# Optimization experiments

Measured on AMD Instinct MI355X. Metric: run time of the kernel, lower is better.

The kernel has to match this reference:

```python
import jax, jax.numpy as jnp
import numpy as np

NUM_HEADS = 32
NUM_KV_HEADS = 8
HEAD_DIM = 64
HIDDEN = 2048
EPS = 1e-05
ROPE_THETA = 1000000.0


def _rmsnorm(x, w):
    # x: [..., head_dim]
    var = jnp.mean(x * x, axis=-1, keepdims=True)
    return w * (x * jax.lax.rsqrt(var + EPS))


def _rope(q, k):
    # q,k: [B, h, T, d]
    T, d = q.shape[2], q.shape[3]
    inv_freq = 1.0 / (ROPE_THETA ** (jnp.arange(0, d, 2, dtype=jnp.float32) / d))
    t = jnp.arange(T, dtype=jnp.float32)
    freqs = jnp.outer(t, inv_freq)               # [T, d/2]
    emb = jnp.concatenate([freqs, freqs], -1)    # [T, d]
    cos = jnp.cos(emb)[None, None].astype(q.dtype)
    sin = jnp.sin(emb)[None, None].astype(q.dtype)

    def rotate(x):
        x1, x2 = x[..., : d // 2], x[..., d // 2 :]
        return jnp.concatenate([-x2, x1], -1)

    return q * cos + rotate(q) * sin, k * cos + rotate(k) * sin


def setup_inputs() -> dict:
    key = jax.random.key(0)
    ks = jax.random.split(key, 7)
    s = 0.02
    x = jax.random.normal(ks[0], (2, 2048, HIDDEN), jnp.float32)
    Wq = jax.random.normal(ks[1], (HIDDEN, NUM_HEADS * HEAD_DIM), jnp.float32) * s
    Wk = jax.random.normal(ks[2], (HIDDEN, NUM_KV_HEADS * HEAD_DIM), jnp.float32) * s
    Wv = jax.random.normal(ks[3], (HIDDEN, NUM_KV_HEADS * HEAD_DIM), jnp.float32) * s
    Wo = jax.random.normal(ks[4], (NUM_HEADS * HEAD_DIM, HIDDEN), jnp.float32) * s
    q_ln_w = jnp.ones((HEAD_DIM,), jnp.float32)
    k_ln_w = jnp.ones((HEAD_DIM,), jnp.float32)
    return {"x": x, "Wq": Wq, "Wk": Wk, "Wv": Wv, "Wo": Wo, "q_ln_w": q_ln_w, "k_ln_w": k_ln_w}


def reference(x, Wq, Wk, Wv, Wo, q_ln_w, k_ln_w):
    B, T, _ = x.shape
    g = NUM_HEADS // NUM_KV_HEADS  # GQA groups = 4
    q = (x @ Wq).reshape(B, T, NUM_HEADS, HEAD_DIM)
    k = (x @ Wk).reshape(B, T, NUM_KV_HEADS, HEAD_DIM)
    v = (x @ Wv).reshape(B, T, NUM_KV_HEADS, HEAD_DIM)
    q = _rmsnorm(q, q_ln_w)
    k = _rmsnorm(k, k_ln_w)
    q = q.transpose(0, 2, 1, 3)  # [B, nh, T, d]
    k = k.transpose(0, 2, 1, 3)  # [B, nkv, T, d]
    v = v.transpose(0, 2, 1, 3)
    q, k = _rope(q, k)
    # native GQA: fold query heads into (kv_head, group) without repeating K/V
    qg = q.reshape(B, NUM_KV_HEADS, g, T, HEAD_DIM)
    scale = 1.0 / jnp.sqrt(jnp.array(HEAD_DIM, q.dtype))
    scores = jnp.einsum("bkgtd,bksd->bkgts", qg, k) * scale  # [B,nkv,g,T,T]
    causal = jnp.tril(jnp.ones((T, T), bool))
    scores = jnp.where(causal, scores, jnp.finfo(scores.dtype).min)
    probs = jax.nn.softmax(scores, axis=-1)
    out = jnp.einsum("bkgts,bksd->bkgtd", probs, v)  # [B,nkv,g,T,d]
    out = out.reshape(B, NUM_HEADS, T, HEAD_DIM).transpose(0, 2, 1, 3).reshape(B, T, -1)
    return out @ Wo
```

## Files before the change

kernel.cpp:

```cpp
#include <hip/hip_runtime.h>
#include <cstdint>
#include <cstddef>

typedef unsigned short u16;
typedef __attribute__((ext_vector_type(8))) short short8;
typedef __attribute__((ext_vector_type(4))) short short4v;
typedef __attribute__((ext_vector_type(4))) float float4v;
typedef __attribute__((ext_vector_type(4))) unsigned short ushort4v;
typedef __attribute__((ext_vector_type(2))) float float2v;

__device__ __forceinline__ u16 f2bf(float f) {
    union { float f; uint32_t u; } x; x.f = f;
    uint32_t r = x.u + 0x7fffu + ((x.u >> 16) & 1u);
    return (u16)(r >> 16);
}
__device__ __forceinline__ uint32_t pack_bf16x2(float lo, float hi) {
    union { float f; uint32_t u; } a, b; a.f = lo; b.f = hi;
    return __builtin_amdgcn_perm(b.u + 0x8000u, a.u + 0x8000u, 0x07060302u);
}
__device__ __forceinline__ void gl_lds16(const u16* g, u16* l) {
    __builtin_amdgcn_global_load_lds(
        (const __attribute__((address_space(1))) void*)g,
        (__attribute__((address_space(3))) void*)l, 16, 0, 0);
}

__global__ __launch_bounds__(256) void prep(const float4v* __restrict__ x,
                                            const float* __restrict__ Wq,
                                            const float* __restrict__ Wk,
                                            const float* __restrict__ Wv,
                                            const float* __restrict__ Wo,
                                            ushort4v* __restrict__ xb,
                                            u16* __restrict__ wqkv_t,
                                            u16* __restrict__ wo_t,
                                            float2v* __restrict__ tab) {
    __shared__ float lds[32][33];
    const int bid = blockIdx.x;
    const int tid = threadIdx.x;
    if (bid < 8192) {
        const int i = bid * 256 + tid;
        float4v v = x[i];
        ushort4v o;
        #pragma unroll
        for (int j = 0; j < 4; ++j) o[j] = f2bf(v[j]);
        xb[i] = o;
        return;
    }
    if (bid < 8448) {
        const int idx = (bid - 8192) * 256 + tid;
        const int t = idx >> 5;
        const int i = idx & 31;
        const float invf = exp2f(-(float)i * (19.931568569324174f / 32.0f));
        float sv, cv;
        sincosf((float)t * invf, &sv, &cv);
        float2v o; o[0] = cv; o[1] = sv;
        tab[idx] = o;
        return;
    }
    const float* src;
    int Ns, n0, k0, scol0;
    u16* dst;
    if (bid < 14592) {
        const int id = bid - 8448;
        const int bx = id % 96, by = id / 96;
        n0 = bx * 32; k0 = by * 32;
        if (n0 < 2048)      { src = Wq; Ns = 2048; scol0 = n0; }
        else if (n0 < 2560) { src = Wk; Ns = 512;  scol0 = n0 - 2048; }
        else                { src = Wv; Ns = 512;  scol0 = n0 - 2560; }
        dst = wqkv_t;
    } else {
        const int id = bid - 14592;
        const int bx = id & 63, by = id >> 6;
        n0 = bx * 32; k0 = by * 32;
        src = Wo; Ns = 2048; scol0 = n0;
        dst = wo_t;
    }
    const int row = tid >> 3;
    const int c4  = (tid & 7) * 4;
    const float4v v = *(const float4v*)(src + (size_t)(k0 + row) * Ns + scol0 + c4);
    #pragma unroll
    for (int i = 0; i < 4; ++i) lds[row][c4 + i] = v[i];
    __syncthreads();
    const int nrow = tid >> 3;
    const int k4   = (tid & 7) * 4;
    ushort4v o;
    #pragma unroll
    for (int i = 0; i < 4; ++i) o[i] = f2bf(lds[k4 + i][nrow]);
    *(ushort4v*)(dst + (size_t)(n0 + nrow) * 2048 + k0 + k4) = o;
}

__global__ __launch_bounds__(256, 3) void gemm_bt(const u16* __restrict__ A,
                                                  const u16* __restrict__ Bt,
                                                  float* __restrict__ C,
                                                  int M, int N, int K) {
    __shared__ u16 lds_a[128 * 32];
    __shared__ u16 lds_b[128 * 32];
    const int tid  = threadIdx.x;
    const int wave = tid >> 6;
    const int lane = tid & 63;
    const int quad = lane >> 4;
    const int l15  = lane & 15;
    const long m0 = (long)blockIdx.x * 128;
    const long n0 = (long)blockIdx.y * 128;
    const int wm = (wave >> 1) * 64;
    const int wn = (wave & 1) * 64;
    const int s_row = tid >> 2;
    const int s_col = (tid & 3) * 8;

    float4v acc[4][4];
    #pragma unroll
    for (int i = 0; i < 4; ++i)
        #pragma unroll
        for (int j = 0; j < 4; ++j)
            #pragma unroll
            for (int r = 0; r < 4; ++r) acc[i][j][r] = 0.0f;

    const u16* ga0 = A  + (m0 + s_row) * (long)K + s_col;
    const u16* ga1 = ga0 + 64 * (long)K;
    const u16* gb0 = Bt + (n0 + s_row) * (long)K + s_col;
    const u16* gb1 = gb0 + 64 * (long)K;
    u16* la = lds_a + tid * 8;
    u16* lb = lds_b + tid * 8;

    const int n_k = K >> 5;
    for (int it = 0; it < n_k; ++it) {
        const int k0 = it << 5;
        gl_lds16(ga0 + k0, la);
        gl_lds16(ga1 + k0, la + 2048);
        gl_lds16(gb0 + k0, lb);
        gl_lds16(gb1 + k0, lb + 2048);
        __syncthreads();
        short8 af[4], bfr[4];
        #pragma unroll
        for (int mt = 0; mt < 4; ++mt)
            af[mt] = *(const short8*)(lds_a + (wm + mt * 16 + l15) * 32 + quad * 8);
        #pragma unroll
        for (int nt = 0; nt < 4; ++nt)
            bfr[nt] = *(const short8*)(lds_b + (wn + nt * 16 + l15) * 32 + quad * 8);
        #pragma unroll
        for (int mt = 0; mt < 4; ++mt)
            #pragma unroll
            for (int nt = 0; nt < 4; ++nt)
                acc[mt][nt] = __builtin_amdgcn_mfma_f32_16x16x32_bf16(af[mt], bfr[nt], acc[mt][nt], 0, 0, 0);
        __syncthreads();
    }
    #pragma unroll
    for (int mt = 0; mt < 4; ++mt) {
        #pragma unroll
        for (int nt = 0; nt < 4; ++nt) {
            const long gr = m0 + wm + mt * 16 + quad * 4;
            const long gc = n0 + wn + nt * 16 + l15;
            #pragma unroll
            for (int r = 0; r < 4; ++r)
                C[(gr + r) * N + gc] = acc[mt][nt][r];
        }
    }
}

__global__ __launch_bounds__(256, 3) void gemm_qkv(const u16* __restrict__ A,
                                                   const u16* __restrict__ Bt,
                                                   const float* __restrict__ qw,
                                                   const float* __restrict__ kw,
                                                   const float2v* __restrict__ tab,
                                                   u16* __restrict__ Qr,
                                                   u16* __restrict__ Kr,
                                                   u16* __restrict__ Vt) {
    const int K = 2048;
    __shared__ u16 lds_a[128 * 32];
    __shared__ u16 lds_b[128 * 32];
    const int tid  = threadIdx.x;
    const int wave = tid >> 6;
    const int lane = tid & 63;
    const int quad = lane >> 4;
    const int l15  = lane & 15;
    const long m0 = (long)blockIdx.x * 128;
    const long n0 = (long)blockIdx.y * 128;
    const int wm = (wave >> 1) * 64;
    const int wn = (wave & 1) * 64;
    const int s_row = tid >> 2;
    const int s_col = (tid & 3) * 8;

    float4v acc[4][4];
    #pragma unroll
    for (int i = 0; i < 4; ++i)
        #pragma unroll
        for (int j = 0; j < 4; ++j)
            #pragma unroll
            for (int r = 0; r < 4; ++r) acc[i][j][r] = 0.0f;

    const u16* ga0 = A  + (m0 + s_row) * (long)K + s_col;
    const u16* ga1 = ga0 + 64 * (long)K;
    const u16* gb0 = Bt + (n0 + s_row) * (long)K + s_col;
    const u16* gb1 = gb0 + 64 * (long)K;
    u16* la = lds_a + tid * 8;
    u16* lb = lds_b + tid * 8;

    const int n_k = K >> 5;
    for (int it = 0; it < n_k; ++it) {
        const int k0 = it << 5;
        gl_lds16(ga0 + k0, la);
        gl_lds16(ga1 + k0, la + 2048);
        gl_lds16(gb0 + k0, lb);
        gl_lds16(gb1 + k0, lb + 2048);
        __syncthreads();
        short8 af[4], bfr[4];
        #pragma unroll
        for (int mt = 0; mt < 4; ++mt)
            af[mt] = *(const short8*)(lds_a + (wm + mt * 16 + l15) * 32 + quad * 8);
        #pragma unroll
        for (int nt = 0; nt < 4; ++nt)
            bfr[nt] = *(const short8*)(lds_b + (wn + nt * 16 + l15) * 32 + quad * 8);
        #pragma unroll
        for (int mt = 0; mt < 4; ++mt)
            #pragma unroll
            for (int nt = 0; nt < 4; ++nt)
                acc[mt][nt] = __builtin_amdgcn_mfma_f32_16x16x32_bf16(af[mt], bfr[nt], acc[mt][nt], 0, 0, 0);
        __syncthreads();
    }

    const int col0 = (int)n0 + wn;
    if (col0 < 2560) {
        const bool isQ = (col0 < 2048);
        const float* lw = isQ ? qw : kw;
        float wreg[4];
        #pragma unroll
        for (int nt = 0; nt < 4; ++nt) wreg[nt] = lw[nt * 16 + l15];
        const float qs = isQ ? 0.18033688011112042f : 1.0f;
        u16* dst = isQ ? (Qr + ((size_t)(col0 >> 6)) * 2048 * 64)
                       : (Kr + ((size_t)((col0 - 2048) >> 6)) * 2048 * 64);
        const size_t head_stride = isQ ? ((size_t)32 * 2048 * 64) : ((size_t)8 * 2048 * 64);
        #pragma unroll
        for (int mt = 0; mt < 4; ++mt) {
            const int gr0 = (int)m0 + wm + mt * 16 + quad * 4;
            const int b = gr0 >> 11, tt0 = gr0 & 2047;
            float rms[4];
            #pragma unroll
            for (int r = 0; r < 4; ++r) {
                float s = 0.0f;
                #pragma unroll
                for (int nt = 0; nt < 4; ++nt) s += acc[mt][nt][r] * acc[mt][nt][r];
                s += __shfl_xor(s, 1);
                s += __shfl_xor(s, 2);
                s += __shfl_xor(s, 4);
                s += __shfl_xor(s, 8);
                rms[r] = rsqrtf(s * (1.0f / 64.0f) + 1e-5f);
            }
            u16* rowp = dst + (size_t)b * head_stride + (size_t)tt0 * 64;
            #pragma unroll
            for (int nt = 0; nt < 2; ++nt) {
                const int i = nt * 16 + l15;
                #pragma unroll
                for (int r = 0; r < 4; ++r) {
                    const float2v cs = tab[(tt0 + r) * 32 + i];
                    const float v1 = acc[mt][nt][r]     * rms[r] * wreg[nt];
                    const float v2 = acc[mt][nt + 2][r] * rms[r] * wreg[nt + 2];
                    const float o1 = (v1 * cs[0] - v2 * cs[1]) * qs;
                    const float o2 = (v2 * cs[0] + v1 * cs[1]) * qs;
                    rowp[(size_t)r * 64 + i]      = f2bf(o1);
                    rowp[(size_t)r * 64 + i + 32] = f2bf(o2);
                }
            }
        }
    } else {
        const int kh = (col0 - 2560) >> 6;
        #pragma unroll
        for (int mt = 0; mt < 4; ++mt) {
            const int gr0 = (int)m0 + wm + mt * 16 + quad * 4;
            const int b = gr0 >> 11, tt0 = gr0 & 2047;
            #pragma unroll
            for (int nt = 0; nt < 4; ++nt) {
                const int d = nt * 16 + l15;
                ushort4v o;
                #pragma unroll
                for (int r = 0; r < 4; ++r) o[r] = f2bf(acc[mt][nt][r]);
                *(ushort4v*)(Vt + (((size_t)(b * 8 + kh)) * 64 + d) * 2048 + tt0) = o;
            }
        }
    }
}

#define KSTR 72
#define VSTR 136
__global__ __launch_bounds__(512, 4) void attn_fwd(const u16* __restrict__ Qr,
                                                   const u16* __restrict__ Kr,
                                                   const u16* __restrict__ Vt,
                                                   u16* __restrict__ Ob) {
    __shared__ u16 lds_k[2][128 * KSTR];
    __shared__ u16 lds_vt[2][64 * VSTR];
    const int tid  = threadIdx.x;
    const int wave = tid >> 6;
    const int lane = tid & 63;
    const int quad = lane >> 4;
    const int l15  = lane & 15;
    const int qxB = blockIdx.y;
    const int qxA = 15 - qxB;
    const int bh = blockIdx.x;
    const int b = bh >> 5, h = bh & 31;
    const int kh = h >> 2;
    const u16* Qh = Qr + ((size_t)(b * 32 + h))  * 2048 * 64;
    const u16* Kh = Kr + ((size_t)(b * 8 + kh))  * 2048 * 64;
    const u16* Vh = Vt + ((size_t)(b * 8 + kh))  * 64 * 2048;

    const int k_key0 = tid >> 3;
    const int k_d0   = (tid & 7) * 8;
    const int v_d0   = tid >> 4;
    const int v_k8   = (tid & 15) * 8;
    const int t15 = tid & 15;
    const int vka = ((2 * t15) & 3) * 32 + (t15 >> 1) * 4;
    const int vkb = ((2 * t15 + 1) & 3) * 32 + (t15 >> 1) * 4;

    const int qrowA = qxA * 128 + wave * 16 + l15;
    const int qrowB = qxB * 128 + wave * 16 + l15;
    short8 qfA[2], qfB[2];
    #pragma unroll
    for (int ks = 0; ks < 2; ++ks) {
        qfA[ks] = *(const short8*)(Qh + (size_t)qrowA * 64 + ks * 32 + quad * 8);
        qfB[ks] = *(const short8*)(Qh + (size_t)qrowB * 64 + ks * 32 + quad * 8);
    }
    short8 qf0 = qfA[0], qf1 = qfA[1];
    int qrow_cur = qrowA;

    float m_i = -3e38f, l_i = 0.0f;
    float4v Oacc[4];
    #pragma unroll
    for (int dt = 0; dt < 4; ++dt)
        #pragma unroll
        for (int r = 0; r < 4; ++r) Oacc[dt][r] = 0.0f;

    short8 kreg[2], vreg[2];
    #pragma unroll
    for (int i = 0; i < 2; ++i) {
        kreg[i] = *(const short8*)(Kh + (size_t)(k_key0 + i * 64) * 64 + k_d0);
        vreg[i] = *(const short8*)(Vh + (size_t)(v_d0 + i * 32) * 2048 + v_k8);
    }
    #pragma unroll
    for (int i = 0; i < 2; ++i) {
        *(short8*)(lds_k[0] + (k_key0 + i * 64) * KSTR + k_d0) = kreg[i];
        short4v vlo = __builtin_shufflevector(vreg[i], vreg[i], 0, 1, 2, 3);
        short4v vhi = __builtin_shufflevector(vreg[i], vreg[i], 4, 5, 6, 7);
        *(short4v*)(lds_vt[0] + (v_d0 + i * 32) * VSTR + vka) = vlo;
        *(short4v*)(lds_vt[0] + (v_d0 + i * 32) * VSTR + vkb) = vhi;
    }
    __syncthreads();

    const int n_it = 17;
    for (int i = 0; i < n_it; ++i) {
        const int p = i & 1;
        const bool last = (i == n_it - 1);
        const int kt_cur = (i <= qxA) ? i : (i - qxA - 1);
        const int kt0 = kt_cur << 7;

        if (!last) {
            const int ip1 = i + 1;
            const int ktn = (ip1 <= qxA) ? ip1 : (ip1 - qxA - 1);
            const size_t nk0 = (size_t)(ktn << 7);
            #pragma unroll
            for (int j = 0; j < 2; ++j) {
                kreg[j] = *(const short8*)(Kh + (nk0 + k_key0 + j * 64) * 64 + k_d0);
                vreg[j] = *(const short8*)(Vh + (size_t)(v_d0 + j * 32) * 2048 + nk0 + v_k8);
            }
        }

        float4v S[8];
        #pragma unroll
        for (int nt = 0; nt < 8; ++nt)
            #pragma unroll
            for (int r = 0; r < 4; ++r) S[nt][r] = 0.0f;
        __builtin_amdgcn_s_setprio(1);
        #pragma unroll
        for (int ks = 0; ks < 2; ++ks) {
            const short8 qf = ks ? qf1 : qf0;
            #pragma unroll
            for (int nt = 0; nt < 8; ++nt) {
                short8 kf = *(const short8*)(lds_k[p] + (nt * 16 + l15) * KSTR + ks * 32 + quad * 8);
                S[nt] = __builtin_amdgcn_mfma_f32_16x16x32_bf16(kf, qf, S[nt], 0, 0, 0);
            }
        }
        __builtin_amdgcn_s_setprio(0);
        if (i == qxA || last) {
            #pragma unroll
            for (int nt = 0; nt < 8; ++nt) {
                const int keyb = kt0 + nt * 16 + quad * 4;
                #pragma unroll
                for (int r = 0; r < 4; ++r)
                    if (keyb + r > qrow_cur) S[nt][r] = -3e38f;
            }
        }
        float mx = S[0][0];
        #pragma unroll
        for (int nt = 0; nt < 8; ++nt)
            #pragma unroll
            for (int r = 0; r < 4; ++r) mx = fmaxf(mx, S[nt][r]);
        mx = fmaxf(mx, __shfl_xor(mx, 16));
        mx = fmaxf(mx, __shfl_xor(mx, 32));
        const float mnew = fmaxf(m_i, mx);
        const float alpha = __builtin_amdgcn_exp2f(m_i - mnew);
        m_i = mnew;
        float rs = 0.0f;
        #pragma unroll
        for (int nt = 0; nt < 8; ++nt)
            #pragma unroll
            for (int r = 0; r < 4; ++r) {
                const float pv = __builtin_amdgcn_exp2f(S[nt][r] - mnew);
                S[nt][r] = pv;
                rs += pv;
            }
        rs += __shfl_xor(rs, 16);
        rs += __shfl_xor(rs, 32);
        l_i = l_i * alpha + rs;
        #pragma unroll
        for (int dt = 0; dt < 4; ++dt)
            #pragma unroll
            for (int r = 0; r < 4; ++r) Oacc[dt][r] *= alpha;

        __builtin_amdgcn_s_setprio(1);
        #pragma unroll
        for (int nt2 = 0; nt2 < 4; ++nt2) {
            union { uint32_t u[2]; short4v s; } p0, p1;
            p0.u[0] = pack_bf16x2(S[2 * nt2][0], S[2 * nt2][1]);
            p0.u[1] = pack_bf16x2(S[2 * nt2][2], S[2 * nt2][3]);
            p1.u[0] = pack_bf16x2(S[2 * nt2 + 1][0], S[2 * nt2 + 1][1]);
            p1.u[1] = pack_bf16x2(S[2 * nt2 + 1][2], S[2 * nt2 + 1][3]);
            #pragma unroll
            for (int dt = 0; dt < 4; ++dt) {
                short8 vv = *(const short8*)(lds_vt[p] + (dt * 16 + l15) * VSTR + quad * 32 + nt2 * 8);
                short4v vlo = __builtin_shufflevector(vv, vv, 0, 1, 2, 3);
                short4v vhi = __builtin_shufflevector(vv, vv, 4, 5, 6, 7);
                Oacc[dt] = __builtin_amdgcn_mfma_f32_16x16x16bf16_1k(vlo, p0.s, Oacc[dt], 0, 0, 0);
                Oacc[dt] = __builtin_amdgcn_mfma_f32_16x16x16bf16_1k(vhi, p1.s, Oacc[dt], 0, 0, 0);
            }
        }
        __builtin_amdgcn_s_setprio(0);

        if (i == qxA) {
            const float rl = 1.0f / l_i;
            #pragma unroll
            for (int dt = 0; dt < 4; ++dt) {
                ushort4v o;
                #pragma unroll
                for (int r = 0; r < 4; ++r) o[r] = f2bf(Oacc[dt][r] * rl);
                *(ushort4v*)(Ob + ((size_t)(b * 2048 + qrowA)) * 2048 + h * 64 + dt * 16 + quad * 4) = o;
            }
            m_i = -3e38f;
            l_i = 0.0f;
            #pragma unroll
            for (int dt = 0; dt < 4; ++dt)
                #pragma unroll
                for (int r = 0; r < 4; ++r) Oacc[dt][r] = 0.0f;
            qf0 = qfB[0];
            qf1 = qfB[1];
            qrow_cur = qrowB;
        }

        if (!last) {
            #pragma unroll
            for (int j = 0; j < 2; ++j) {
                *(short8*)(lds_k[1 - p] + (k_key0 + j * 64) * KSTR + k_d0) = kreg[j];
                short4v vlo = __builtin_shufflevector(vreg[j], vreg[j], 0, 1, 2, 3);
                short4v vhi = __builtin_shufflevector(vreg[j], vreg[j], 4, 5, 6, 7);
                *(short4v*)(lds_vt[1 - p] + (v_d0 + j * 32) * VSTR + vka) = vlo;
                *(short4v*)(lds_vt[1 - p] + (v_d0 + j * 32) * VSTR + vkb) = vhi;
            }
        }
        __syncthreads();
    }
    const float rl = 1.0f / l_i;
    #pragma unroll
    for (int dt = 0; dt < 4; ++dt) {
        ushort4v o;
        #pragma unroll
        for (int r = 0; r < 4; ++r) o[r] = f2bf(Oacc[dt][r] * rl);
        *(ushort4v*)(Ob + ((size_t)(b * 2048 + qrowB)) * 2048 + h * 64 + dt * 16 + quad * 4) = o;
    }
}

extern "C" void kernel_launch(void* const* d_in, const int* in_sizes, int n_in,
                              void* d_out, int out_size, void* d_ws, size_t ws_size,
                              hipStream_t stream) {
    (void)in_sizes; (void)n_in; (void)out_size; (void)ws_size;
    const float* x  = (const float*)d_in[0];
    const float* Wq = (const float*)d_in[1];
    const float* Wk = (const float*)d_in[2];
    const float* Wv = (const float*)d_in[3];
    const float* Wo = (const float*)d_in[4];
    const float* qw = (const float*)d_in[5];
    const float* kw = (const float*)d_in[6];
    float* out = (float*)d_out;

    char* ws = (char*)d_ws;
    size_t off = 0;
    auto alloc = [&](size_t bytes) {
        char* p = ws + off;
        off += (bytes + 255) & ~(size_t)255;
        return p;
    };
    u16* xb     = (u16*)alloc((size_t)8388608 * 2);
    u16* wqkv_t = (u16*)alloc((size_t)3072 * 2048 * 2);
    u16* wo_t   = (u16*)alloc((size_t)2048 * 2048 * 2);
    u16* q_r    = (u16*)alloc((size_t)2 * 32 * 2048 * 64 * 2);
    u16* k_r    = (u16*)alloc((size_t)2 * 8 * 2048 * 64 * 2);
    u16* v_r    = (u16*)alloc((size_t)2 * 8 * 64 * 2048 * 2);
    float2v* rtab = (float2v*)alloc((size_t)2048 * 32 * 8);
    u16* attnb  = xb;

    hipLaunchKernelGGL(prep, dim3(18688), dim3(256), 0, stream,
                       (const float4v*)x, Wq, Wk, Wv, Wo,
                       (ushort4v*)xb, wqkv_t, wo_t, rtab);
    hipLaunchKernelGGL(gemm_qkv, dim3(32, 24), dim3(256), 0, stream,
                       xb, wqkv_t, qw, kw, rtab, q_r, k_r, v_r);
    hipLaunchKernelGGL(attn_fwd, dim3(64, 8), dim3(512), 0, stream, q_r, k_r, v_r, attnb);
    hipLaunchKernelGGL(gemm_bt, dim3(32, 16), dim3(256), 0, stream,
                       attnb, wo_t, out, 4096, 2048, 2048);
}
```

Before: 289.0 us.

## Stage K/V via direct global-to-LDS loads with XOR swizzle and two Q tiles per wave

The QKV GEMM epilogue now writes K and V in an XOR-swizzled layout. This lets the attention kernel copy tiles straight into unpadded LDS with global_load_lds and read them back without bank conflicts, replacing the old register round-trip with padded strides. The attention block shrinks to 4 waves, and each wave handles 32 query rows (two 16-row tiles), so every K/V fragment read from LDS feeds twice as many MFMAs. The cost is higher register pressure from the doubled accumulators and softmax state, and a tighter coupling between the swizzle the producer writes and the one the consumer reads.

```diff
diff --git a/kernel.cpp b/kernel.cpp
--- a/kernel.cpp
+++ b/kernel.cpp
@@ -225,6 +225,7 @@
         #pragma unroll
         for (int nt = 0; nt < 4; ++nt) wreg[nt] = lw[nt * 16 + l15];
         const float qs = isQ ? 0.18033688011112042f : 1.0f;
+        const int swm = isQ ? 0 : 7;
         u16* dst = isQ ? (Qr + ((size_t)(col0 >> 6)) * 2048 * 64)
                        : (Kr + ((size_t)((col0 - 2048) >> 6)) * 2048 * 64);
         const size_t head_stride = isQ ? ((size_t)32 * 2048 * 64) : ((size_t)8 * 2048 * 64);
@@ -255,8 +256,11 @@
                     const float v2 = acc[mt][nt + 2][r] * rms[r] * wreg[nt + 2];
                     const float o1 = (v1 * cs[0] - v2 * cs[1]) * qs;
                     const float o2 = (v2 * cs[0] + v1 * cs[1]) * qs;
-                    rowp[(size_t)r * 64 + i]      = f2bf(o1);
-                    rowp[(size_t)r * 64 + i + 32] = f2bf(o2);
+                    const int k7 = (tt0 + r) & swm;
+                    const int i1 = (((i >> 3) ^ k7) << 3) | (i & 7);
+                    const int i2 = ((((i + 32) >> 3) ^ k7) << 3) | (i & 7);
+                    rowp[(size_t)r * 64 + i1] = f2bf(o1);
+                    rowp[(size_t)r * 64 + i2] = f2bf(o2);
                 }
             }
         }
@@ -266,31 +270,84 @@
         for (int mt = 0; mt < 4; ++mt) {
             const int gr0 = (int)m0 + wm + mt * 16 + quad * 4;
             const int b = gr0 >> 11, tt0 = gr0 & 2047;
+            const int tb = tt0 & ~127;
+            const int tl = tt0 & 127;
+            const int p0b = ((tl & 15) >> 2) * 32 + (tl >> 4) * 4;
             #pragma unroll
             for (int nt = 0; nt < 4; ++nt) {
                 const int d = nt * 16 + l15;
                 ushort4v o;
                 #pragma unroll
                 for (int r = 0; r < 4; ++r) o[r] = f2bf(acc[mt][nt][r]);
-                *(ushort4v*)(Vt + (((size_t)(b * 8 + kh)) * 64 + d) * 2048 + tt0) = o;
-            }
-        }
-    }
-}
-
-#define KSTR 72
-#define VSTR 136
-__global__ __launch_bounds__(512, 4) void attn_fwd(const u16* __restrict__ Qr,
+                const int col = tb + ((((p0b >> 3) ^ (d & 7)) << 3) | (p0b & 7));
+                *(ushort4v*)(Vt + (((size_t)(b * 8 + kh)) * 64 + d) * 2048 + col) = o;
+            }
+        }
+    }
+}
+
+#define SOFTMAX_PACK(S, m_i, l_i, O, pf)                                    \
+    {                                                                       \
+        float mx = S[0][0];                                                 \
+        _Pragma("unroll")                                                   \
+        for (int nt = 0; nt < 8; ++nt)                                      \
+            _Pragma("unroll")                                               \
+            for (int r = 0; r < 4; ++r) mx = fmaxf(mx, S[nt][r]);           \
+        mx = fmaxf(mx, __shfl_xor(mx, 16));                                 \
+        mx = fmaxf(mx, __shfl_xor(mx, 32));                                 \
+        const float mnew = fmaxf(m_i, mx);                                  \
+        const float alpha = __builtin_amdgcn_exp2f(m_i - mnew);             \
+        m_i = mnew;                                                         \
+        float rs = 0.0f;                                                    \
+        _Pragma("unroll")                                                   \
+        for (int nt = 0; nt < 8; ++nt)                                      \
+            _Pragma("unroll")                                               \
+            for (int r = 0; r < 4; ++r) {                                   \
+                const float pv = __builtin_amdgcn_exp2f(S[nt][r] - mnew);   \
+                S[nt][r] = pv;                                              \
+                rs += pv;                                                   \
+            }                                                               \
+        rs += __shfl_xor(rs, 16);                                           \
+        rs += __shfl_xor(rs, 32);                                           \
+        l_i = l_i * alpha + rs;                                             \
+        _Pragma("unroll")                                                   \
+        for (int dt = 0; dt < 4; ++dt)                                      \
+            _Pragma("unroll")                                               \
+            for (int r = 0; r < 4; ++r) O[dt][r] *= alpha;                  \
+        _Pragma("unroll")                                                   \
+        for (int nt = 0; nt < 8; ++nt) {                                    \
+            union { uint32_t u[2]; short4v s; } pu;                         \
+            pu.u[0] = pack_bf16x2(S[nt][0], S[nt][1]);                      \
+            pu.u[1] = pack_bf16x2(S[nt][2], S[nt][3]);                      \
+            pf[nt] = pu.s;                                                  \
+        }                                                                   \
+    }
+
+#define WRITE_O(O, l_i, qrow)                                               \
+    {                                                                       \
+        const float rl = 1.0f / l_i;                                        \
+        _Pragma("unroll")                                                   \
+        for (int dt = 0; dt < 4; ++dt) {                                    \
+            ushort4v o;                                                     \
+            _Pragma("unroll")                                               \
+            for (int r = 0; r < 4; ++r) o[r] = f2bf(O[dt][r] * rl);         \
+            *(ushort4v*)(Ob + ((size_t)(b * 2048 + (qrow))) * 2048 +        \
+                         h * 64 + dt * 16 + quad * 4) = o;                  \
+        }                                                                   \
+    }
+
+__global__ __launch_bounds__(256, 2) void attn_fwd(const u16* __restrict__ Qr,
                                                    const u16* __restrict__ Kr,
                                                    const u16* __restrict__ Vt,
                                                    u16* __restrict__ Ob) {
-    __shared__ u16 lds_k[2][128 * KSTR];
-    __shared__ u16 lds_vt[2][64 * VSTR];
+    __shared__ u16 lds_k[2][128 * 64];
+    __shared__ u16 lds_v[2][64 * 128];
     const int tid  = threadIdx.x;
     const int wave = tid >> 6;
     const int lane = tid & 63;
     const int quad = lane >> 4;
     const int l15  = lane & 15;
+    const int sw7  = l15 & 7;
     const int qxB = blockIdx.y;
     const int qxA = 15 - qxB;
     const int bh = blockIdx.x;
@@ -300,46 +357,36 @@
     const u16* Kh = Kr + ((size_t)(b * 8 + kh))  * 2048 * 64;
     const u16* Vh = Vt + ((size_t)(b * 8 + kh))  * 64 * 2048;
 
-    const int k_key0 = tid >> 3;
-    const int k_d0   = (tid & 7) * 8;
-    const int v_d0   = tid >> 4;
-    const int v_k8   = (tid & 15) * 8;
-    const int t15 = tid & 15;
-    const int vka = ((2 * t15) & 3) * 32 + (t15 >> 1) * 4;
-    const int vkb = ((2 * t15 + 1) & 3) * 32 + (t15 >> 1) * 4;
-
-    const int qrowA = qxA * 128 + wave * 16 + l15;
-    const int qrowB = qxB * 128 + wave * 16 + l15;
-    short8 qfA[2], qfB[2];
+    const int w32 = wave * 32;
+    int qrow_c0 = qxA * 128 + w32 + l15;
+    int qrow_c1 = qrow_c0 + 16;
+    short8 qf[2][2];
     #pragma unroll
     for (int ks = 0; ks < 2; ++ks) {
-        qfA[ks] = *(const short8*)(Qh + (size_t)qrowA * 64 + ks * 32 + quad * 8);
-        qfB[ks] = *(const short8*)(Qh + (size_t)qrowB * 64 + ks * 32 + quad * 8);
-    }
-    short8 qf0 = qfA[0], qf1 = qfA[1];
-    int qrow_cur = qrowA;
-
-    float m_i = -3e38f, l_i = 0.0f;
-    float4v Oacc[4];
+        qf[0][ks] = *(const short8*)(Qh + (size_t)qrow_c0 * 64 + ks * 32 + quad * 8);
+        qf[1][ks] = *(const short8*)(Qh + (size_t)qrow_c1 * 64 + ks * 32 + quad * 8);
+    }
+
+    float m0v = -3e38f, l0v = 0.0f, m1v = -3e38f, l1v = 0.0f;
+    float4v O0[4], O1[4];
     #pragma unroll
     for (int dt = 0; dt < 4; ++dt)
         #pragma unroll
-        for (int r = 0; r < 4; ++r) Oacc[dt][r] = 0.0f;
-
-    short8 kreg[2], vreg[2];
-    #pragma unroll
-    for (int i = 0; i < 2; ++i) {
-        kreg[i] = *(const short8*)(Kh + (size_t)(k_key0 + i * 64) * 64 + k_d0);
-        vreg[i] = *(const short8*)(Vh + (size_t)(v_d0 + i * 32) * 2048 + v_k8);
-    }
-    #pragma unroll
-    for (int i = 0; i < 2; ++i) {
-        *(short8*)(lds_k[0] + (k_key0 + i * 64) * KSTR + k_d0) = kreg[i];
-        short4v vlo = __builtin_shufflevector(vreg[i], vreg[i], 0, 1, 2, 3);
-        short4v vhi = __builtin_shufflevector(vreg[i], vreg[i], 4, 5, 6, 7);
-        *(short4v*)(lds_vt[0] + (v_d0 + i * 32) * VSTR + vka) = vlo;
-        *(short4v*)(lds_vt[0] + (v_d0 + i * 32) * VSTR + vkb) = vhi;
-    }
+        for (int r = 0; r < 4; ++r) { O0[dt][r] = 0.0f; O1[dt][r] = 0.0f; }
+
+    const int vrow = tid >> 4;
+    const int vchk = (tid & 15) * 8;
+    auto stage = [&](int pb, int k0) {
+        #pragma unroll
+        for (int j = 0; j < 4; ++j)
+            gl_lds16(Kh + (size_t)k0 * 64 + (j * 256 + tid) * 8,
+                     &lds_k[pb][(j * 256 + tid) * 8]);
+        #pragma unroll
+        for (int j = 0; j < 4; ++j)
+            gl_lds16(Vh + (size_t)(j * 16 + vrow) * 2048 + k0 + vchk,
+                     &lds_v[pb][(j * 256 + tid) * 8]);
+    };
+    stage(0, 0);
     __syncthreads();
 
     const int n_it = 17;
@@ -352,125 +399,80 @@
         if (!last) {
             const int ip1 = i + 1;
             const int ktn = (ip1 <= qxA) ? ip1 : (ip1 - qxA - 1);
-            const size_t nk0 = (size_t)(ktn << 7);
-            #pragma unroll
-            for (int j = 0; j < 2; ++j) {
-                kreg[j] = *(const short8*)(Kh + (nk0 + k_key0 + j * 64) * 64 + k_d0);
-                vreg[j] = *(const short8*)(Vh + (size_t)(v_d0 + j * 32) * 2048 + nk0 + v_k8);
-            }
-        }
-
-        float4v S[8];
+            stage(1 - p, ktn << 7);
+        }
+
+        float4v S0[8], S1[8];
         #pragma unroll
         for (int nt = 0; nt < 8; ++nt)
             #pragma unroll
-            for (int r = 0; r < 4; ++r) S[nt][r] = 0.0f;
+            for (int r = 0; r < 4; ++r) { S0[nt][r] = 0.0f; S1[nt][r] = 0.0f; }
         __builtin_amdgcn_s_setprio(1);
         #pragma unroll
         for (int ks = 0; ks < 2; ++ks) {
-            const short8 qf = ks ? qf1 : qf0;
             #pragma unroll
             for (int nt = 0; nt < 8; ++nt) {
-                short8 kf = *(const short8*)(lds_k[p] + (nt * 16 + l15) * KSTR + ks * 32 + quad * 8);
-                S[nt] = __builtin_amdgcn_mfma_f32_16x16x32_bf16(kf, qf, S[nt], 0, 0, 0);
+                short8 kf = *(const short8*)(lds_k[p] + (nt * 16 + l15) * 64 +
+                                             (((ks * 4 + quad) ^ sw7) << 3));
+                S0[nt] = __builtin_amdgcn_mfma_f32_16x16x32_bf16(kf, qf[0][ks], S0[nt], 0, 0, 0);
+                S1[nt] = __builtin_amdgcn_mfma_f32_16x16x32_bf16(kf, qf[1][ks], S1[nt], 0, 0, 0);
             }
         }
         __builtin_amdgcn_s_setprio(0);
+
         if (i == qxA || last) {
             #pragma unroll
             for (int nt = 0; nt < 8; ++nt) {
                 const int keyb = kt0 + nt * 16 + quad * 4;
                 #pragma unroll
-                for (int r = 0; r < 4; ++r)
-                    if (keyb + r > qrow_cur) S[nt][r] = -3e38f;
-            }
-        }
-        float mx = S[0][0];
-        #pragma unroll
-        for (int nt = 0; nt < 8; ++nt)
-            #pragma unroll
-            for (int r = 0; r < 4; ++r) mx = fmaxf(mx, S[nt][r]);
-        mx = fmaxf(mx, __shfl_xor(mx, 16));
-        mx = fmaxf(mx, __shfl_xor(mx, 32));
-        const float mnew = fmaxf(m_i, mx);
-        const float alpha = __builtin_amdgcn_exp2f(m_i - mnew);
-        m_i = mnew;
-        float rs = 0.0f;
-        #pragma unroll
-        for (int nt = 0; nt < 8; ++nt)
-            #pragma unroll
-            for (int r = 0; r < 4; ++r) {
-                const float pv = __builtin_amdgcn_exp2f(S[nt][r] - mnew);
-                S[nt][r] = pv;
-                rs += pv;
-            }
-        rs += __shfl_xor(rs, 16);
-        rs += __shfl_xor(rs, 32);
-        l_i = l_i * alpha + rs;
-        #pragma unroll
-        for (int dt = 0; dt < 4; ++dt)
-            #pragma unroll
-            for (int r = 0; r < 4; ++r) Oacc[dt][r] *= alpha;
+                for (int r = 0; r < 4; ++r) {
+                    if (keyb + r > qrow_c0) S0[nt][r] = -3e38f;
+                    if (keyb + r > qrow_c1) S1[nt][r] = -3e38f;
+                }
+            }
+        }
+
+        short4v pf0[8], pf1[8];
+        SOFTMAX_PACK(S0, m0v, l0v, O0, pf0);
+        SOFTMAX_PACK(S1, m1v, l1v, O1, pf1);
 
         __builtin_amdgcn_s_setprio(1);
         #pragma unroll
         for (int nt2 = 0; nt2 < 4; ++nt2) {
-            union { uint32_t u[2]; short4v s; } p0, p1;
-            p0.u[0] = pack_bf16x2(S[2 * nt2][0], S[2 * nt2][1]);
-            p0.u[1] = pack_bf16x2(S[2 * nt2][2], S[2 * nt2][3]);
-            p1.u[0] = pack_bf16x2(S[2 * nt2 + 1][0], S[2 * nt2 + 1][1]);
-            p1.u[1] = pack_bf16x2(S[2 * nt2 + 1][2], S[2 * nt2 + 1][3]);
             #pragma unroll
             for (int dt = 0; dt < 4; ++dt) {
-                short8 vv = *(const short8*)(lds_vt[p] + (dt * 16 + l15) * VSTR + quad * 32 + nt2 * 8);
+                short8 vv = *(const short8*)(lds_v[p] + (dt * 16 + l15) * 128 +
+                                             (((quad * 4 + nt2) ^ sw7) << 3));
                 short4v vlo = __builtin_shufflevector(vv, vv, 0, 1, 2, 3);
                 short4v vhi = __builtin_shufflevector(vv, vv, 4, 5, 6, 7);
-                Oacc[dt] = __builtin_amdgcn_mfma_f32_16x16x16bf16_1k(vlo, p0.s, Oacc[dt], 0, 0, 0);
-                Oacc[dt] = __builtin_amdgcn_mfma_f32_16x16x16bf16_1k(vhi, p1.s, Oacc[dt], 0, 0, 0);
+                O0[dt] = __builtin_amdgcn_mfma_f32_16x16x16bf16_1k(vlo, pf0[2 * nt2],     O0[dt], 0, 0, 0);
+                O0[dt] = __builtin_amdgcn_mfma_f32_16x16x16bf16_1k(vhi, pf0[2 * nt2 + 1], O0[dt], 0, 0, 0);
+                O1[dt] = __builtin_amdgcn_mfma_f32_16x16x16bf16_1k(vlo, pf1[2 * nt2],     O1[dt], 0, 0, 0);
+                O1[dt] = __builtin_amdgcn_mfma_f32_16x16x16bf16_1k(vhi, pf1[2 * nt2 + 1], O1[dt], 0, 0, 0);
             }
         }
         __builtin_amdgcn_s_setprio(0);
 
         if (i == qxA) {
-            const float rl = 1.0f / l_i;
-            #pragma unroll
-            for (int dt = 0; dt < 4; ++dt) {
-                ushort4v o;
-                #pragma unroll
-                for (int r = 0; r < 4; ++r) o[r] = f2bf(Oacc[dt][r] * rl);
-                *(ushort4v*)(Ob + ((size_t)(b * 2048 + qrowA)) * 2048 + h * 64 + dt * 16 + quad * 4) = o;
-            }
-            m_i = -3e38f;
-            l_i = 0.0f;
+            WRITE_O(O0, l0v, qrow_c0);
+            WRITE_O(O1, l1v, qrow_c1);
+            m0v = -3e38f; l0v = 0.0f; m1v = -3e38f; l1v = 0.0f;
             #pragma unroll
             for (int dt = 0; dt < 4; ++dt)
                 #pragma unroll
-                for (int r = 0; r < 4; ++r) Oacc[dt][r] = 0.0f;
-            qf0 = qfB[0];
-            qf1 = qfB[1];
-            qrow_cur = qrowB;
-        }
-
-        if (!last) {
-            #pragma unroll
-            for (int j = 0; j < 2; ++j) {
-                *(short8*)(lds_k[1 - p] + (k_key0 + j * 64) * KSTR + k_d0) = kreg[j];
-                short4v vlo = __builtin_shufflevector(vreg[j], vreg[j], 0, 1, 2, 3);
-                short4v vhi = __builtin_shufflevector(vreg[j], vreg[j], 4, 5, 6, 7);
-                *(short4v*)(lds_vt[1 - p] + (v_d0 + j * 32) * VSTR + vka) = vlo;
-                *(short4v*)(lds_vt[1 - p] + (v_d0 + j * 32) * VSTR + vkb) = vhi;
+                for (int r = 0; r < 4; ++r) { O0[dt][r] = 0.0f; O1[dt][r] = 0.0f; }
+            qrow_c0 = qxB * 128 + w32 + l15;
+            qrow_c1 = qrow_c0 + 16;
+            #pragma unroll
+            for (int ks = 0; ks < 2; ++ks) {
+                qf[0][ks] = *(const short8*)(Qh + (size_t)qrow_c0 * 64 + ks * 32 + quad * 8);
+                qf[1][ks] = *(const short8*)(Qh + (size_t)qrow_c1 * 64 + ks * 32 + quad * 8);
             }
         }
         __syncthreads();
     }
-    const float rl = 1.0f / l_i;
-    #pragma unroll
-    for (int dt = 0; dt < 4; ++dt) {
-        ushort4v o;
-        #pragma unroll
-        for (int r = 0; r < 4; ++r) o[r] = f2bf(Oacc[dt][r] * rl);
-        *(ushort4v*)(Ob + ((size_t)(b * 2048 + qrowB)) * 2048 + h * 64 + dt * 16 + quad * 4) = o;
-    }
+    WRITE_O(O0, l0v, qrow_c0);
+    WRITE_O(O1, l1v, qrow_c1);
 }
 
 extern "C" void kernel_launch(void* const* d_in, const int* in_sizes, int n_in,
@@ -507,7 +509,7 @@
                        (ushort4v*)xb, wqkv_t, wo_t, rtab);
     hipLaunchKernelGGL(gemm_qkv, dim3(32, 24), dim3(256), 0, stream,
                        xb, wqkv_t, qw, kw, rtab, q_r, k_r, v_r);
-    hipLaunchKernelGGL(attn_fwd, dim3(64, 8), dim3(512), 0, stream, q_r, k_r, v_r, attnb);
+    hipLaunchKernelGGL(attn_fwd, dim3(64, 8), dim3(256), 0, stream, q_r, k_r, v_r, attnb);
     hipLaunchKernelGGL(gemm_bt, dim3(32, 16), dim3(256), 0, stream,
                        attnb, wo_t, out, 4096, 2048, 2048);
 }
```

Measured after the change: 288.5 us. About the same (-0.2%).
